# Kernel optimization log

Hardware: AMD Instinct MI355X
Metric: run time of the kernel (lower is better)

The kernel has to match this reference:

```python
import jax, jax.numpy as jnp
import numpy as np

N, D, H, O = 2048, 128, 256, 1  # batch, input_dim, hidden_dim, output_dim
LN_EPS = 1e-5


def setup_inputs() -> dict:
    key = jax.random.key(0)
    ks = jax.random.split(key, 10)
    s = lambda fan_in: 1.0 / np.sqrt(fan_in)
    return {
        "array": jax.random.normal(ks[0], (N, D), dtype=jnp.float32),
        # per-feature Linear(1, H) stacked: weight [D, H], bias [D, H]
        "W_in": jax.random.uniform(ks[1], (D, H), jnp.float32, -1.0, 1.0),
        "b_in": jax.random.uniform(ks[2], (D, H), jnp.float32, -1.0, 1.0),
        # FactorAttentionLayer (width D): W: Linear(D, D), V: Linear(D, 1), LayerNorm(D)
        "Wf": jax.random.uniform(ks[3], (D, D), jnp.float32, -s(D), s(D)),
        "bf": jax.random.uniform(ks[4], (D,), jnp.float32, -s(D), s(D)),
        "Vf": jax.random.uniform(ks[5], (D,), jnp.float32, -s(D), s(D)),
        "bv": jnp.zeros((), jnp.float32),
        "ln_g": jnp.ones((D,), jnp.float32),
        "ln_b": jnp.zeros((D,), jnp.float32),
        # fc_hidden: Linear(D*H, H); fc_output: Linear(H, O)  (stored as [in, out])
        "Wh": jax.random.uniform(ks[6], (D * H, H), jnp.float32, -s(D * H), s(D * H)),
        "bh": jax.random.uniform(ks[7], (H,), jnp.float32, -s(D * H), s(D * H)),
        "Wo": jax.random.uniform(ks[8], (H, O), jnp.float32, -s(H), s(H)),
        "bo": jax.random.uniform(ks[9], (O,), jnp.float32, -s(H), s(H)),
    }


def reference(array, W_in, b_in, Wf, bf, Vf, bv, ln_g, ln_b, Wh, bh, Wo, bo):
    # Fused per-feature Linear(1,H)+ReLU: [n, D, H]
    p = jax.nn.relu(array[:, :, None] * W_in[None] + b_in[None])
    # permute(0, 2, 1) -> [n, H, D]
    x = jnp.transpose(p, (0, 2, 1))
    # FactorAttention: tanh-linear, softmax over axis 1 (the H axis), residual mul, LayerNorm over D
    u = jnp.tanh(jnp.einsum('nhd,de->nhe', x, Wf) + bf)          # [n, H, D]
    scores = jnp.einsum('nhd,d->nh', u, Vf) + bv                  # [n, H]
    attn = jax.nn.softmax(scores, axis=1)[:, :, None]             # [n, H, 1]
    y = x + x * attn                                              # [n, H, D]
    mu = jnp.mean(y, axis=-1, keepdims=True)
    var = jnp.mean((y - mu) ** 2, axis=-1, keepdims=True)
    y = (y - mu) * jax.lax.rsqrt(var + LN_EPS) * ln_g + ln_b
    # flatten [n, H*D] and MLP head (dropout = identity in eval)
    xx = y.reshape(y.shape[0], -1)
    h = jax.nn.relu(xx @ Wh + bh)
    return h @ Wo + bo
```

## Files before the change

### kernel.cpp

```cpp
#include <hip/hip_runtime.h>

#define NB 2048
#define DD 128
#define HH 256
#define KF 32768
#define LN_EPS 1e-5f
#define KSPLIT 32
#define KSL (KF / KSPLIT)

typedef __attribute__((ext_vector_type(8))) short short8;
typedef __attribute__((ext_vector_type(4))) float float4_t;
typedef __attribute__((ext_vector_type(4))) float f4;

__device__ __forceinline__ unsigned short f2bf(float f) {
    unsigned int u = __builtin_bit_cast(unsigned int, f);
    u += 0x7fffu + ((u >> 16) & 1u);
    return (unsigned short)(u >> 16);
}

__device__ __forceinline__ unsigned int pkbf(float lo, float hi) {
    unsigned int r;
    asm("v_cvt_pk_bf16_f32 %0, %1, %2" : "=v"(r) : "v"(lo), "v"(hi));
    return r;
}

__device__ __forceinline__ void gl2lds16(const void* g, void* l) {
    __builtin_amdgcn_global_load_lds(
        (const __attribute__((address_space(1))) unsigned int*)g,
        (__attribute__((address_space(3))) unsigned int*)l, 16, 0, 0);
}

__global__ void stats_k(const float* __restrict__ arr, const float* __restrict__ Win,
                        const float* __restrict__ bin, float2* __restrict__ stats,
                        float* __restrict__ WinT, float* __restrict__ binT,
                        float* __restrict__ bias2, float* __restrict__ Cacc) {
    __shared__ float a_s[2][128];
    __shared__ float tile[32][33];
    int bid = blockIdx.x;
    int t = threadIdx.x;

    if (bid >= 1024) {
        if (bid == 1088) { bias2[t] = 0.f; return; }
        if (bid >= 1089) {
            float* p = Cacc + (long)(bid - 1089) * 2048 + t * 8;
            *(f4*)p = (f4){0.f, 0.f, 0.f, 0.f};
            *(f4*)(p + 4) = (f4){0.f, 0.f, 0.f, 0.f};
            return;
        }
        int tid = bid - 1024;
        int mat = tid >> 5;
        int dt = (tid >> 3) & 3;
        int ht = tid & 7;
        const float* src = mat ? bin : Win;
        float* dst = mat ? binT : WinT;
        int c = t & 31, r = t >> 5;
#pragma unroll
        for (int rr = r; rr < 32; rr += 8)
            tile[rr][c] = src[(dt * 32 + rr) * 256 + ht * 32 + c];
        __syncthreads();
#pragma unroll
        for (int rr = r; rr < 32; rr += 8)
            dst[(ht * 32 + rr) * 128 + dt * 32 + c] = tile[c][rr];
        return;
    }

    int n0 = bid * 2;
    if (t < 256) a_s[t >> 7][t & 127] = arr[n0 * 128 + t];
    __syncthreads();
    int h = t;
    float sum[2] = {0.f, 0.f}, ssq[2] = {0.f, 0.f};
    for (int d = 0; d < 128; ++d) {
        float w = Win[d * 256 + h];
        float bb = bin[d * 256 + h];
#pragma unroll
        for (int q = 0; q < 2; ++q) {
            float x = fmaxf(fmaf(a_s[q][d], w, bb), 0.f);
            sum[q] += x;
            ssq[q] = fmaf(x, x, ssq[q]);
        }
    }
#pragma unroll
    for (int q = 0; q < 2; ++q) {
        float mu = sum[q] * (1.f / 128.f);
        float var = fmaxf(ssq[q] * (1.f / 128.f) - mu * mu, 0.f);
        float rs = rsqrtf(var + LN_EPS);
        stats[(long)(n0 + q) * HH + h] = make_float2(rs, mu * rs);
    }
}

__global__ void prep_b(const float* __restrict__ Wh, const float* __restrict__ g,
                       const float* __restrict__ beta, unsigned short* __restrict__ WhbT,
                       float* __restrict__ bias2) {
    __shared__ unsigned short tile[64][65];
    __shared__ float red[4][64];
    int kb = blockIdx.x;
    int jb = blockIdx.y;
    int t = threadIdx.x;
    int c = t & 63, r4 = t >> 6;
    int k0 = kb * 64;
    float bsum = 0.f;
    for (int rr = r4; rr < 64; rr += 4) {
        int k = k0 + rr, d = k & 127;
        float v = Wh[(long)k * 256 + jb * 64 + c];
        tile[rr][c] = f2bf(g[d] * v);
        bsum = fmaf(beta[d], v, bsum);
    }
    __syncthreads();
    for (int rr = r4; rr < 64; rr += 4)
        WhbT[(long)(jb * 64 + rr) * KF + k0 + c] = tile[c][rr];
    red[r4][c] = bsum;
    __syncthreads();
    if (r4 == 0)
        atomicAdd(&bias2[jb * 64 + c], red[0][c] + red[1][c] + red[2][c] + red[3][c]);
}

__global__ __launch_bounds__(512, 4) void gemm_f(
        const float* __restrict__ arr, const float* __restrict__ WinT,
        const float* __restrict__ binT, const float2* __restrict__ stats,
        const unsigned short* __restrict__ Bt,
        float* __restrict__ Cacc) {
    __shared__ unsigned short Bs[2][256 * 32];
    __shared__ float Ws[8 * 128];
    __shared__ float Vs[8 * 128];
    __shared__ float2 Ss[128 * 9];
    int bid = blockIdx.x;
    int mt = bid & 15;
    int ks = bid >> 4;
    int m0 = mt * 128;
    long k0 = (long)ks * KSL;
    int h0 = ks * 8;
    int t = threadIdx.x;
    int lane = t & 63, wave = t >> 6;
    int wm = (wave >> 1) * 32;
    int wn = (wave & 1) * 128;
    int fr = lane & 15;
    int kch = lane >> 4;
    int fk8 = kch * 8;

    float4_t acc[2][8] = {};

    const unsigned short* Bab = Bt + k0;
    long boff0 = (long)(t >> 2) * KF + (long)(t & 3) * 8;
    long boff1 = boff0 + 128l * KF;

    if (t < 256) {
        *(f4*)&Ws[t * 4] = *(const f4*)(WinT + h0 * 128 + t * 4);
    } else {
        *(f4*)&Vs[(t - 256) * 4] = *(const f4*)(binT + h0 * 128 + (t - 256) * 4);
    }
    {
        int sr = t >> 2, sc = (t & 3) * 2;
        const float2* sp = stats + (long)(m0 + sr) * HH + h0 + sc;
        float2 v0 = sp[0], v1 = sp[1];
        Ss[sr * 9 + sc] = v0;
        Ss[sr * 9 + sc + 1] = v1;
    }
    gl2lds16(Bab + boff0, &Bs[0][t * 8]);
    gl2lds16(Bab + boff1, &Bs[0][(t + 512) * 8]);

    int row0 = m0 + wm + fr;
    f4 aa[2][2];
    __syncthreads();

    for (int it = 0; it < 32; ++it) {
        int q = it >> 3, hl = it & 7, cur = it & 1;
        if (it < 31) {
            int itn = it + 1;
            int kap = (itn & 7) * 128 + (itn >> 3) * 32;
            gl2lds16(Bab + kap + boff0, &Bs[cur ^ 1][t * 8]);
            gl2lds16(Bab + kap + boff1, &Bs[cur ^ 1][(t + 512) * 8]);
        }
        if (hl == 0) {
#pragma unroll
            for (int mi = 0; mi < 2; ++mi) {
                const float* ap = arr + (long)(row0 + mi * 16) * DD + q * 32 + fk8;
                aa[mi][0] = *(const f4*)ap;
                aa[mi][1] = *(const f4*)(ap + 4);
            }
        }
        int wb = hl * 128 + q * 32 + fk8;
        f4 w0 = *(const f4*)&Ws[wb], w1 = *(const f4*)&Ws[wb + 4];
        f4 v0 = *(const f4*)&Vs[wb], v1 = *(const f4*)&Vs[wb + 4];
        short8 af[2];
#pragma unroll
        for (int mi = 0; mi < 2; ++mi) {
            float2 sv = Ss[(wm + mi * 16 + fr) * 9 + hl];
            float rs = sv.x, nm = -sv.y;
            float z0 = fmaf(fmaxf(fmaf(aa[mi][0][0], w0[0], v0[0]), 0.f), rs, nm);
            float z1 = fmaf(fmaxf(fmaf(aa[mi][0][1], w0[1], v0[1]), 0.f), rs, nm);
            float z2 = fmaf(fmaxf(fmaf(aa[mi][0][2], w0[2], v0[2]), 0.f), rs, nm);
            float z3 = fmaf(fmaxf(fmaf(aa[mi][0][3], w0[3], v0[3]), 0.f), rs, nm);
            float z4 = fmaf(fmaxf(fmaf(aa[mi][1][0], w1[0], v1[0]), 0.f), rs, nm);
            float z5 = fmaf(fmaxf(fmaf(aa[mi][1][1], w1[1], v1[1]), 0.f), rs, nm);
            float z6 = fmaf(fmaxf(fmaf(aa[mi][1][2], w1[2], v1[2]), 0.f), rs, nm);
            float z7 = fmaf(fmaxf(fmaf(aa[mi][1][3], w1[3], v1[3]), 0.f), rs, nm);
            union { short8 s; unsigned int u[4]; } pk;
            pk.u[0] = pkbf(z0, z1);
            pk.u[1] = pkbf(z2, z3);
            pk.u[2] = pkbf(z4, z5);
            pk.u[3] = pkbf(z6, z7);
            af[mi] = pk.s;
        }
#pragma unroll
        for (int half = 0; half < 2; ++half) {
            short8 bfv[4];
#pragma unroll
            for (int n4 = 0; n4 < 4; ++n4) {
                int j = wn + (half * 4 + n4) * 16 + fr;
                bfv[n4] = *(const short8*)&Bs[cur][j * 32 + fk8];
            }
#pragma unroll
            for (int mi = 0; mi < 2; ++mi)
#pragma unroll
                for (int n4 = 0; n4 < 4; ++n4)
                    acc[mi][half * 4 + n4] = __builtin_amdgcn_mfma_f32_16x16x32_bf16(
                        af[mi], bfv[n4], acc[mi][half * 4 + n4], 0, 0, 0);
        }
        if (it < 31) __syncthreads();
    }

    int rb = (lane >> 4) * 4;
#pragma unroll
    for (int mi = 0; mi < 2; ++mi) {
#pragma unroll
        for (int ni = 0; ni < 8; ++ni) {
            int n = wn + ni * 16 + fr;
#pragma unroll
            for (int r = 0; r < 4; ++r) {
                int m = m0 + wm + mi * 16 + rb + r;
                atomicAdd(&Cacc[(long)m * 256 + n], acc[mi][ni][r]);
            }
        }
    }
}

__global__ void finale(const float* __restrict__ Cacc, const float* __restrict__ bh,
                       const float* __restrict__ Wo, const float* __restrict__ bo,
                       const float* __restrict__ bias2, float* __restrict__ out) {
    __shared__ float red[4];
    int n = blockIdx.x, t = threadIdx.x;
    int lane = t & 63, wave = t >> 6;
    float s = bh[t] + bias2[t] + Cacc[(long)n * 256 + t];
    float v = fmaxf(s, 0.f) * Wo[t];
#pragma unroll
    for (int o = 32; o; o >>= 1) v += __shfl_down(v, o);
    if (lane == 0) red[wave] = v;
    __syncthreads();
    if (t == 0) out[n] = red[0] + red[1] + red[2] + red[3] + bo[0];
}

extern "C" void kernel_launch(void* const* d_in, const int* in_sizes, int n_in,
                              void* d_out, int out_size, void* d_ws, size_t ws_size,
                              hipStream_t stream) {
    const float* arr  = (const float*)d_in[0];
    const float* Win  = (const float*)d_in[1];
    const float* bin  = (const float*)d_in[2];
    const float* ln_g = (const float*)d_in[7];
    const float* ln_b = (const float*)d_in[8];
    const float* Wh   = (const float*)d_in[9];
    const float* bh   = (const float*)d_in[10];
    const float* Wo   = (const float*)d_in[11];
    const float* bo   = (const float*)d_in[12];
    float* out = (float*)d_out;

    char* ws = (char*)d_ws;
    unsigned short* WhbT = (unsigned short*)ws;
    float2* stats = (float2*)(ws + 16777216ull);
    float* Cacc   = (float*)(ws + 20971520ull);
    float* WinT   = (float*)(ws + 23068672ull);
    float* binT   = (float*)(ws + 23199744ull);
    float* bias2  = (float*)(ws + 23330816ull);

    hipLaunchKernelGGL(stats_k, dim3(1345), dim3(256), 0, stream,
                       arr, Win, bin, stats, WinT, binT, bias2, Cacc);
    hipLaunchKernelGGL(prep_b, dim3(512, 4), dim3(256), 0, stream,
                       Wh, ln_g, ln_b, WhbT, bias2);
    hipLaunchKernelGGL(gemm_f, dim3(512), dim3(512), 0, stream,
                       arr, WinT, binT, stats, WhbT, Cacc);
    hipLaunchKernelGGL(finale, dim3(NB), dim3(256), 0, stream,
                       Cacc, bh, Wo, bo, bias2, out);
}
```

Baseline: 222.9 us.

## Replace split-K atomic accumulation with per-slice partial buffers reduced in finale

The GEMM no longer atomically adds its split-K partial results into a shared accumulator; each of the 32 K-slices writes its own 2048x256 partial buffer with plain stores, and the final kernel sums the 32 slices per output element. This removes the zero-initialisation of the accumulator and the contended float atomics. Block indices are also remapped so that the K-slices sharing an XCD are grouped, to improve L2 reuse of the B operand. The cost is 64 MB of extra partial-buffer traffic that the finale must read back.

```diff
diff --git a/kernel.cpp b/kernel.cpp
--- a/kernel.cpp
+++ b/kernel.cpp
@@ -33,7 +33,7 @@
 __global__ void stats_k(const float* __restrict__ arr, const float* __restrict__ Win,
                         const float* __restrict__ bin, float2* __restrict__ stats,
                         float* __restrict__ WinT, float* __restrict__ binT,
-                        float* __restrict__ bias2, float* __restrict__ Cacc) {
+                        float* __restrict__ bias2) {
     __shared__ float a_s[2][128];
     __shared__ float tile[32][33];
     int bid = blockIdx.x;
@@ -41,12 +41,6 @@
 
     if (bid >= 1024) {
         if (bid == 1088) { bias2[t] = 0.f; return; }
-        if (bid >= 1089) {
-            float* p = Cacc + (long)(bid - 1089) * 2048 + t * 8;
-            *(f4*)p = (f4){0.f, 0.f, 0.f, 0.f};
-            *(f4*)(p + 4) = (f4){0.f, 0.f, 0.f, 0.f};
-            return;
-        }
         int tid = bid - 1024;
         int mat = tid >> 5;
         int dt = (tid >> 3) & 3;
@@ -118,14 +112,16 @@
         const float* __restrict__ arr, const float* __restrict__ WinT,
         const float* __restrict__ binT, const float2* __restrict__ stats,
         const unsigned short* __restrict__ Bt,
-        float* __restrict__ Cacc) {
+        float* __restrict__ Cp) {
     __shared__ unsigned short Bs[2][256 * 32];
     __shared__ float Ws[8 * 128];
     __shared__ float Vs[8 * 128];
     __shared__ float2 Ss[128 * 9];
     int bid = blockIdx.x;
-    int mt = bid & 15;
-    int ks = bid >> 4;
+    int xcd = bid & 7;
+    int idx = bid >> 3;
+    int ks = xcd * 4 + (idx >> 4);
+    int mt = idx & 15;
     int m0 = mt * 128;
     long k0 = (long)ks * KSL;
     int h0 = ks * 8;
@@ -220,6 +216,7 @@
     }
 
     int rb = (lane >> 4) * 4;
+    float* Cb = Cp + (long)ks * NB * 256;
 #pragma unroll
     for (int mi = 0; mi < 2; ++mi) {
 #pragma unroll
@@ -228,19 +225,21 @@
 #pragma unroll
             for (int r = 0; r < 4; ++r) {
                 int m = m0 + wm + mi * 16 + rb + r;
-                atomicAdd(&Cacc[(long)m * 256 + n], acc[mi][ni][r]);
+                Cb[(long)m * 256 + n] = acc[mi][ni][r];
             }
         }
     }
 }
 
-__global__ void finale(const float* __restrict__ Cacc, const float* __restrict__ bh,
+__global__ void finale(const float* __restrict__ Cp, const float* __restrict__ bh,
                        const float* __restrict__ Wo, const float* __restrict__ bo,
                        const float* __restrict__ bias2, float* __restrict__ out) {
     __shared__ float red[4];
     int n = blockIdx.x, t = threadIdx.x;
     int lane = t & 63, wave = t >> 6;
-    float s = bh[t] + bias2[t] + Cacc[(long)n * 256 + t];
+    float s = bh[t] + bias2[t];
+    for (int sl = 0; sl < KSPLIT; ++sl)
+        s += Cp[(long)sl * NB * 256 + (long)n * 256 + t];
     float v = fmaxf(s, 0.f) * Wo[t];
 #pragma unroll
     for (int o = 32; o; o >>= 1) v += __shfl_down(v, o);
@@ -266,17 +265,17 @@
     char* ws = (char*)d_ws;
     unsigned short* WhbT = (unsigned short*)ws;
     float2* stats = (float2*)(ws + 16777216ull);
-    float* Cacc   = (float*)(ws + 20971520ull);
-    float* WinT   = (float*)(ws + 23068672ull);
-    float* binT   = (float*)(ws + 23199744ull);
-    float* bias2  = (float*)(ws + 23330816ull);
-
-    hipLaunchKernelGGL(stats_k, dim3(1345), dim3(256), 0, stream,
-                       arr, Win, bin, stats, WinT, binT, bias2, Cacc);
+    float* Cp     = (float*)(ws + 20971520ull);
+    float* WinT   = (float*)(ws + 88080384ull);
+    float* binT   = (float*)(ws + 88211456ull);
+    float* bias2  = (float*)(ws + 88342528ull);
+
+    hipLaunchKernelGGL(stats_k, dim3(1089), dim3(256), 0, stream,
+                       arr, Win, bin, stats, WinT, binT, bias2);
     hipLaunchKernelGGL(prep_b, dim3(512, 4), dim3(256), 0, stream,
                        Wh, ln_g, ln_b, WhbT, bias2);
     hipLaunchKernelGGL(gemm_f, dim3(512), dim3(512), 0, stream,
-                       arr, WinT, binT, stats, WhbT, Cacc);
+                       arr, WinT, binT, stats, WhbT, Cp);
     hipLaunchKernelGGL(finale, dim3(NB), dim3(256), 0, stream,
-                       Cacc, bh, Wo, bo, bias2, out);
-}
+                       Cp, bh, Wo, bo, bias2, out);
+}
```

Result: faster. 196.2 us (-12.0%).
